# Performance work log

Hardware: AMD Instinct MI355X
Metric: run time of the kernel (lower is better)

Reference implementation:

```python
import jax, jax.numpy as jnp
import numpy as np

# Sizes: N nodes, E edges, C channels (atoms/node), CF channel_nf, R relations,
# H hidden/feature dim (uniform across the 2 AM_EGCL layers), L layers.
N, E, C, CF, R, H, L = 10000, 160000, 4, 16, 7, 256, 2
EPS = 1e-5


def setup_inputs() -> dict:
    key = jax.random.key(0)
    ks = jax.random.split(key, 16)
    p = lambda k, shape: (jax.random.normal(k, shape, jnp.float32) * 0.02)
    inp = {
        "input": jax.random.normal(ks[0], (N, H), jnp.float32),
        "coords": jax.random.normal(ks[1], (N, C, 3), jnp.float32),
        "channel_attr": jax.random.normal(ks[2], (N, C, CF), jnp.float32),
        # strictly positive channel weights (atom-occupancy style)
        "channel_weights": jax.random.uniform(ks[3], (N, C), jnp.float32) + 0.5,
        "edge_weights": jax.random.uniform(ks[4], (E,), jnp.float32),
    }
    src = jax.random.randint(ks[5], (E,), 0, N)
    dst = jax.random.randint(ks[6], (E,), 0, N)
    rel = jax.random.randint(ks[7], (E,), 0, R)
    inp["edge_list"] = jnp.stack([src, dst, rel], axis=1)
    ein = 2 * H + CF + 2 * CF  # h_i, h_j, radial feat, pooled channel attr i/j
    inp.update({
        "W_rad": p(ks[8], (L, C * C, CF)), "b_rad": jnp.zeros((L, CF), jnp.float32),
        "W_e1": p(ks[9], (L, ein, H)), "b_e1": jnp.zeros((L, H), jnp.float32),
        "W_e2": p(ks[10], (L, H, H)), "b_e2": jnp.zeros((L, H), jnp.float32),
        "W_c1": p(ks[11], (L, H, H)), "b_c1": jnp.zeros((L, H), jnp.float32),
        "W_c2": p(ks[12], (L, H, C * C)),
        "W_n1": p(ks[13], (L, R * H + H, H)), "b_n1": jnp.zeros((L, H), jnp.float32),
        "W_n2": p(ks[14], (L, H, H)), "b_n2": jnp.zeros((L, H), jnp.float32),
        "ln_g": jnp.ones((L, H), jnp.float32), "ln_b": jnp.zeros((L, H), jnp.float32),
    })
    return inp


def _am_egcl(h, x, edge_list, channel_attr, channel_weights, edge_weights, prm):
    """One adaptive multichannel equivariant graph conv layer."""
    (W_rad, b_rad, W_e1, b_e1, W_e2, b_e2, W_c1, b_c1, W_c2,
     W_n1, b_n1, W_n2, b_n2, ln_g, ln_b) = prm
    row, col, rel = edge_list[:, 0], edge_list[:, 1], edge_list[:, 2]
    # --- multichannel invariant radial features -------------------------------
    xd = x[row][:, :, None, :] - x[col][:, None, :, :]        # [E,C,C,3]
    radial = jnp.sum(xd * xd, axis=-1)                         # [E,C,C]
    wmask = channel_weights[row][:, :, None] * channel_weights[col][:, None, :]
    radial = radial * wmask
    rad_feat = jax.nn.silu(radial.reshape(-1, C * C) @ W_rad + b_rad)  # [E,CF]
    # pooled (weighted-mean) channel attribute per node
    csum = jnp.sum(channel_weights, axis=-1, keepdims=True)
    ca = jnp.sum(channel_attr * channel_weights[..., None], axis=1) / csum  # [N,CF]
    # --- edge message MLP ------------------------------------------------------
    m_in = jnp.concatenate([h[row], h[col], rad_feat, ca[row], ca[col]], axis=-1)
    m = jax.nn.silu(jax.nn.silu(m_in @ W_e1 + b_e1) @ W_e2 + b_e2)  # [E,H]
    m = m * edge_weights[:, None]
    # --- equivariant coord update ---------------------------------------------
    phi = (jax.nn.silu(m @ W_c1 + b_c1) @ W_c2).reshape(-1, C, C)   # [E,C,C]
    trans = jnp.mean(xd * phi[..., None], axis=2)                   # [E,C,3]
    ones = jnp.ones((trans.shape[0],), x.dtype)
    cnt = jnp.maximum(jax.ops.segment_sum(ones, row, num_segments=N), 1.0)
    x_out = x + jax.ops.segment_sum(trans, row, num_segments=N) / cnt[:, None, None]
    # --- relational node aggregation (GearNet-style, per-relation bins) --------
    seg = col * R + rel
    agg = jax.ops.segment_sum(m, seg, num_segments=N * R).reshape(N, R * H)
    h_out = jax.nn.silu(jnp.concatenate([agg, h], axis=-1) @ W_n1 + b_n1) @ W_n2 + b_n2
    # dropout p=0 (eval) -> identity; then LayerNorm
    mu = jnp.mean(h_out, axis=-1, keepdims=True)
    var = jnp.var(h_out, axis=-1, keepdims=True)
    h_out = (h_out - mu) * jax.lax.rsqrt(var + EPS) * ln_g + ln_b
    return h_out, x_out


def reference(input, edge_list, coords, channel_attr, channel_weights, edge_weights,
              W_rad, b_rad, W_e1, b_e1, W_e2, b_e2, W_c1, b_c1, W_c2,
              W_n1, b_n1, W_n2, b_n2, ln_g, ln_b):
    h, x = input, coords
    for i in range(L):  # fixed small layer count
        prm = (W_rad[i], b_rad[i], W_e1[i], b_e1[i], W_e2[i], b_e2[i],
               W_c1[i], b_c1[i], W_c2[i], W_n1[i], b_n1[i], W_n2[i], b_n2[i],
               ln_g[i], ln_b[i])
        h, x = _am_egcl(h, x, edge_list, channel_attr, channel_weights,
                        edge_weights, prm)
    return h, x  # (node_feature [N,H], coord_feature [N,C,3])
```

## Files before the change

### kernel.cpp

```cpp
#include <hip/hip_runtime.h>
#include <hip/hip_bf16.h>

#define NN 10000
#define EE 160000
#define CCH 4
#define CF 16
#define RR 7
#define HH 256
#define NSEG 70000
#define SCB 274
#define EPSV 1e-5f

typedef unsigned short ushort_t;
typedef __bf16 bf16x8 __attribute__((ext_vector_type(8)));
typedef float f32x4 __attribute__((ext_vector_type(4)));

__device__ __forceinline__ float silu_f(float v) {
    float e = __builtin_amdgcn_exp2f(v * -1.442695040888963f);
    return v * __builtin_amdgcn_rcpf(1.f + e);
}

__device__ __forceinline__ ushort_t bf16u_m(float f) {
    unsigned int u = __builtin_bit_cast(unsigned int, f);
    u += 0x7fffu + ((u >> 16) & 1u);
    return (ushort_t)(u >> 16);
}

__device__ __forceinline__ ushort_t bf16u_n(float f) {
    return __builtin_bit_cast(ushort_t, (__bf16)f);
}

__device__ __forceinline__ float ubf2f(ushort_t u) {
    unsigned int v = ((unsigned int)u) << 16;
    return __builtin_bit_cast(float, v);
}


__device__ __forceinline__ void pack_tile(
    const float* __restrict__ W, ushort_t* __restrict__ out,
    int Kreal, int N, int kt, int nt, int NTOT, int lane)
{
    int n = nt * 16 + (lane & 15);
    int kbase = kt * 32 + (lane >> 4) * 8;
    ushort_t* o = out + ((size_t)(kt * NTOT + nt) * 64 + lane) * 8;
    #pragma unroll
    for (int j = 0; j < 8; ++j) {
        int k = kbase + j;
        o[j] = (k < Kreal) ? bf16u_n(W[(size_t)k * N + n]) : (ushort_t)0;
    }
}

__device__ __forceinline__ void pack_ab_tile(
    const float* __restrict__ W_e1, ushort_t* __restrict__ pab,
    int kt, int nt, int lane)
{
    int nl = nt * 16 + (lane & 15);
    int kbase = kt * 32 + (lane >> 4) * 8;
    ushort_t* o = pab + ((size_t)(kt * 32 + nt) * 64 + lane) * 8;
    #pragma unroll
    for (int j = 0; j < 8; ++j) {
        int k = kbase + j;
        float v = 0.f;
        if (k < 256) {
            v = (nl < 256) ? W_e1[(size_t)k * 256 + nl]
                           : W_e1[(size_t)(256 + k) * 256 + (nl - 256)];
        } else if (k < 272) {
            int kk = k - 256;
            v = (nl < 256) ? W_e1[(size_t)(528 + kk) * 256 + nl]
                           : W_e1[(size_t)(544 + kk) * 256 + (nl - 256)];
        }
        o[j] = bf16u_n(v);
    }
}

__device__ __forceinline__ void pack_e1c_tile(
    const float* __restrict__ W_e1, ushort_t* __restrict__ pe1c,
    int nt, int lane)
{
    int n = nt * 16 + (lane & 15);
    int kbase = (lane >> 4) * 8;
    ushort_t* o = pe1c + ((size_t)nt * 64 + lane) * 8;
    #pragma unroll
    for (int j = 0; j < 8; ++j) {
        int k = kbase + j;
        o[j] = (k < 16) ? bf16u_n(W_e1[(size_t)(512 + k) * 256 + n]) : (ushort_t)0;
    }
}

__device__ __forceinline__ void pack_dispatch(
    int c, int lane,
    const float* __restrict__ W_e1, const float* __restrict__ W_e2,
    const float* __restrict__ W_c1, const float* __restrict__ W_c2,
    const float* __restrict__ W_n1, const float* __restrict__ W_n2,
    ushort_t* __restrict__ pab, ushort_t* __restrict__ pe1c,
    ushort_t* __restrict__ pe2,
    ushort_t* __restrict__ pc1, ushort_t* __restrict__ pc2,
    ushort_t* __restrict__ pn1, ushort_t* __restrict__ pn2)
{
    int l = 0;
    if (c >= 1720) { l = 1; c -= 1720; }
    const float* We1 = W_e1 + (size_t)l * 143360;
    if (c < 288) {
        pack_ab_tile(We1, pab + (size_t)l * 147456, c / 32, c % 32, lane);
    } else if (c < 304) {
        pack_e1c_tile(We1, pe1c + (size_t)l * 8192, c - 288, lane);
    } else if (c < 432) {
        int d = c - 304;
        pack_tile(W_e2 + (size_t)l * 65536, pe2 + (size_t)l * 65536,
                  256, 256, d / 16, d & 15, 16, lane);
    } else if (c < 560) {
        int d = c - 432;
        pack_tile(W_c1 + (size_t)l * 65536, pc1 + (size_t)l * 65536,
                  256, 256, d / 16, d & 15, 16, lane);
    } else if (c < 568) {
        int d = c - 560;
        pack_tile(W_c2 + (size_t)l * 4096, pc2 + (size_t)l * 4096,
                  256, 16, d, 0, 1, lane);
    } else if (c < 1592) {
        int d = c - 568;
        pack_tile(W_n1 + (size_t)l * 524288, pn1 + (size_t)l * 524288,
                  2048, 256, d / 16, d & 15, 16, lane);
    } else {
        int d = c - 1592;
        pack_tile(W_n2 + (size_t)l * 65536, pn2 + (size_t)l * 65536,
                  256, 256, d / 16, d & 15, 16, lane);
    }
}


__global__ __launch_bounds__(256) void prep_kernel(
    const float* __restrict__ input, ushort_t* __restrict__ hb16,
    const float* __restrict__ attr, const float* __restrict__ cw,
    ushort_t* __restrict__ cab16,
    int* __restrict__ hist, int* __restrict__ cursor,
    float* __restrict__ deg, float* __restrict__ xacc,
    const float* __restrict__ W_e1, const float* __restrict__ W_e2,
    const float* __restrict__ W_c1, const float* __restrict__ W_c2,
    const float* __restrict__ W_n1, const float* __restrict__ W_n2,
    ushort_t* __restrict__ pab, ushort_t* __restrict__ pe1c,
    ushort_t* __restrict__ pe2,
    ushort_t* __restrict__ pc1, ushort_t* __restrict__ pc2,
    ushort_t* __restrict__ pn1, ushort_t* __restrict__ pn2)
{
    int b = blockIdx.x, tid = threadIdx.x;
    if (b < 10000) {
        int t = b * 256 + tid;
        hb16[t] = bf16u_n(input[t]);
    } else if (b < 10625) {
        int t = (b - 10000) * 256 + tid;
        int n = t >> 4, f = t & 15;
        float s = 0.f, cs = 0.f;
        #pragma unroll
        for (int c = 0; c < CCH; ++c) {
            float w = cw[n * CCH + c];
            s  += attr[(n * CCH + c) * CF + f] * w;
            cs += w;
        }
        cab16[t] = bf16u_n(s / cs);
    } else if (b < 10899) {
        int t = (b - 10625) * 256 + tid;
        if (t < NSEG) hist[t] = 0;
    } else if (b < 11173) {
        int t = (b - 10899) * 256 + tid;
        if (t < NSEG) cursor[t] = 0;
    } else if (b < 11213) {
        int t = (b - 11173) * 256 + tid;
        if (t < NN) deg[t] = 0.f;
    } else if (b < 11682) {
        int t = (b - 11213) * 256 + tid;
        if (t < NN * 12) xacc[t] = 0.f;
    } else {
        int c = (b - 11682) * 4 + (tid >> 6);
        pack_dispatch(c, tid & 63, W_e1, W_e2, W_c1, W_c2, W_n1, W_n2,
                      pab, pe1c, pe2, pc1, pc2, pn1, pn2);
    }
}

__global__ __launch_bounds__(256) void histdeg_kernel(
    const int* __restrict__ el, int* __restrict__ hist, float* __restrict__ deg)
{
    int e = blockIdx.x * 256 + threadIdx.x;
    if (e < EE) {
        int r = el[e * 3], c = el[e * 3 + 1], rl = el[e * 3 + 2];
        atomicAdd(&hist[c * RR + rl], 1);
        atomicAdd(&deg[r], 1.f);
    }
}

__global__ __launch_bounds__(256) void scan1_kernel(
    const int* __restrict__ hist, int* __restrict__ pscan, int* __restrict__ bsum)
{
    __shared__ int sc[256];
    int b = blockIdx.x, t = threadIdx.x, i = b * 256 + t;
    int v = (i < NSEG) ? hist[i] : 0;
    sc[t] = v; __syncthreads();
    for (int off = 1; off < 256; off <<= 1) {
        int u = (t >= off) ? sc[t - off] : 0;
        __syncthreads();
        sc[t] += u;
        __syncthreads();
    }
    if (i < NSEG) pscan[i] = sc[t] - v;
    if (t == 255) bsum[b] = sc[255];
}

__global__ __launch_bounds__(256) void scan2_kernel(
    const int* __restrict__ bsum, int* __restrict__ bofs, int nb)
{
    __shared__ int sc[512];
    int t = threadIdx.x;
    int o1 = (t < nb) ? bsum[t] : 0;
    int o2 = (t + 256 < nb) ? bsum[t + 256] : 0;
    sc[t] = o1; sc[t + 256] = o2;
    __syncthreads();
    for (int off = 1; off < 512; off <<= 1) {
        int u1 = (t >= off) ? sc[t - off] : 0;
        int u2 = (t + 256 >= off) ? sc[t + 256 - off] : 0;
        __syncthreads();
        sc[t] += u1; sc[t + 256] += u2;
        __syncthreads();
    }
    if (t < nb) bofs[t] = sc[t] - o1;
    if (t + 256 < nb) bofs[t + 256] = sc[t + 256] - o2;
}

__global__ __launch_bounds__(256) void scan3_kernel(
    const int* __restrict__ pscan, const int* __restrict__ bofs, int* __restrict__ segst)
{
    int b = blockIdx.x, t = threadIdx.x, i = b * 256 + t;
    if (i < NSEG) segst[i] = pscan[i] + bofs[b];
    if (i == 0) segst[NSEG] = EE;
}

__global__ __launch_bounds__(256) void scatter_kernel(
    const int* __restrict__ el, const int* __restrict__ segst,
    int* __restrict__ cursor, int* __restrict__ perm)
{
    int e = blockIdx.x * 256 + threadIdx.x;
    if (e < EE) {
        int s = el[e * 3 + 1] * RR + el[e * 3 + 2];
        int pos = segst[s] + atomicAdd(&cursor[s], 1);
        perm[pos] = e;
    }
}


__global__ __launch_bounds__(256, 3) void abk_kernel(
    const ushort_t* __restrict__ hb16, const ushort_t* __restrict__ cab16,
    const ushort_t* __restrict__ pab, const float* __restrict__ b_e1,
    ushort_t* __restrict__ A16, ushort_t* __restrict__ B16)
{
    __shared__ ushort_t inbuf[32][296];
    __shared__ ushort_t obuf[32][520];
    const int tid = threadIdx.x, lane = tid & 63, w = tid >> 6;
    const int ar = lane & 15, aq = (lane >> 4) * 8, quad = lane >> 4;
    const int n0 = blockIdx.x * 32;
    const uint4 z4 = {0u, 0u, 0u, 0u};

    #pragma unroll
    for (int it = 0; it < 4; ++it) {
        int c = it * 256 + tid;
        int e = c >> 5, i4 = c & 31;
        int node = n0 + e;
        uint4 v = (node < NN) ? ((const uint4*)(hb16 + (size_t)node * 256))[i4] : z4;
        *(uint4*)&inbuf[e][i4 * 8] = v;
    }
    if (tid < 64) {
        int e = tid >> 1, i4 = tid & 1;
        int node = n0 + e;
        uint4 v = (node < NN) ? ((const uint4*)(cab16 + node * 16))[i4] : z4;
        *(uint4*)&inbuf[e][256 + i4 * 8] = v;
    } else if (tid < 128) {
        int c = tid - 64, e = c >> 1, i4 = c & 1;
        *(uint4*)&inbuf[e][272 + i4 * 8] = z4;
    }
    __syncthreads();

    const f32x4 Z = {0.f, 0.f, 0.f, 0.f};
    f32x4 acc[2][8];
    #pragma unroll
    for (int mt = 0; mt < 2; ++mt)
        #pragma unroll
        for (int jt = 0; jt < 8; ++jt) acc[mt][jt] = Z;
    for (int kt = 0; kt < 9; ++kt) {
        bf16x8 a0 = *(const bf16x8*)&inbuf[ar][kt * 32 + aq];
        bf16x8 a1 = *(const bf16x8*)&inbuf[16 + ar][kt * 32 + aq];
        #pragma unroll
        for (int jt = 0; jt < 8; ++jt) {
            bf16x8 b = *(const bf16x8*)(pab + ((size_t)(kt * 32 + w * 8 + jt) * 64 + lane) * 8);
            acc[0][jt] = __builtin_amdgcn_mfma_f32_16x16x32_bf16(a0, b, acc[0][jt], 0, 0, 0);
            acc[1][jt] = __builtin_amdgcn_mfma_f32_16x16x32_bf16(a1, b, acc[1][jt], 0, 0, 0);
        }
    }
    #pragma unroll
    for (int jt = 0; jt < 8; ++jt) {
        int n = w * 128 + jt * 16 + ar;
        float bias = (n < 256) ? b_e1[n] : 0.f;
        #pragma unroll
        for (int mt = 0; mt < 2; ++mt)
            #pragma unroll
            for (int r = 0; r < 4; ++r)
                obuf[mt * 16 + quad * 4 + r][n] = bf16u_n(acc[mt][jt][r] + bias);
    }
    __syncthreads();
    #pragma unroll
    for (int it = 0; it < 8; ++it) {
        int c = it * 256 + tid;
        int e = c >> 6, i4 = c & 63;
        int node = n0 + e;
        if (node < NN) {
            if (i4 < 32)
                *(uint4*)(A16 + (size_t)node * 256 + i4 * 8) = *(const uint4*)&obuf[e][i4 * 8];
            else
                *(uint4*)(B16 + (size_t)node * 256 + (i4 - 32) * 8) = *(const uint4*)&obuf[e][256 + (i4 - 32) * 8];
        }
    }
}


template<int KT, int NTOT>
__device__ __forceinline__ void mfma_stage32(
    const ushort_t (&A)[32][584], int colOff,
    const ushort_t* __restrict__ Wp, int w, int lane,
    f32x4 (&acc)[2][4])
{
    const f32x4 Z = {0.f, 0.f, 0.f, 0.f};
    #pragma unroll
    for (int mt = 0; mt < 2; ++mt)
        #pragma unroll
        for (int j = 0; j < 4; ++j) acc[mt][j] = Z;
    const int ar = lane & 15, aq = (lane >> 4) * 8;
    for (int kt = 0; kt < KT; ++kt) {
        bf16x8 a0 = *(const bf16x8*)&A[ar][colOff + kt * 32 + aq];
        bf16x8 a1 = *(const bf16x8*)&A[16 + ar][colOff + kt * 32 + aq];
        #pragma unroll
        for (int j = 0; j < 4; ++j) {
            bf16x8 b = *(const bf16x8*)(Wp + ((size_t)(kt * NTOT + w * 4 + j) * 64 + lane) * 8);
            acc[0][j] = __builtin_amdgcn_mfma_f32_16x16x32_bf16(a0, b, acc[0][j], 0, 0, 0);
            acc[1][j] = __builtin_amdgcn_mfma_f32_16x16x32_bf16(a1, b, acc[1][j], 0, 0, 0);
        }
    }
}


__global__ __launch_bounds__(256, 4) void edge_kernel(
    const int* __restrict__ el, const int* __restrict__ perm,
    const float* __restrict__ cw,
    const float* __restrict__ ew, const float* __restrict__ x,
    const ushort_t* __restrict__ A16, const ushort_t* __restrict__ B16,
    const float* __restrict__ W_rad, const float* __restrict__ b_rad,
    const ushort_t* __restrict__ pe1c,
    const ushort_t* __restrict__ pe2, const float* __restrict__ b_e2,
    const ushort_t* __restrict__ pc1, const float* __restrict__ b_c1,
    const ushort_t* __restrict__ pc2,
    ushort_t* __restrict__ mb16, float* __restrict__ xacc)
{
    __shared__ ushort_t abuf[32][584];
    __shared__ float radbuf[32][16];
    __shared__ int rowS[32], colS[32];
    __shared__ float ewS[32];

    const int tid = threadIdx.x, lane = tid & 63, w = tid >> 6;
    const int ar = lane & 15, aq = (lane >> 4) * 8, quad = lane >> 4;
    const int e0 = blockIdx.x * 32;

    if (tid < 32) {
        int eg = perm[e0 + tid];
        rowS[tid] = el[eg * 3 + 0];
        colS[tid] = el[eg * 3 + 1];
        ewS[tid]  = ew[eg];
    }
    __syncthreads();

    #pragma unroll
    for (int it = 0; it < 4; ++it) {
        int c = it * 256 + tid;
        int e = c >> 5, i4 = c & 31;
        bf16x8 va = *(const bf16x8*)((const uint4*)(A16 + (size_t)rowS[e] * 256) + i4);
        bf16x8 vb = *(const bf16x8*)((const uint4*)(B16 + (size_t)colS[e] * 256) + i4);
        bf16x8 vs;
        #pragma unroll
        for (int j = 0; j < 8; ++j)
            vs[j] = (__bf16)((float)va[j] + (float)vb[j]);
        *(bf16x8*)&abuf[e][288 + i4 * 8] = vs;
    }
    #pragma unroll
    for (int it = 0; it < 2; ++it) {
        int t = it * 256 + tid;
        int e = t >> 4, ab = t & 15, a = ab >> 2, b = ab & 3;
        int row = rowS[e], col = colS[e];
        float d0 = x[row * 12 + a * 3 + 0] - x[col * 12 + b * 3 + 0];
        float d1 = x[row * 12 + a * 3 + 1] - x[col * 12 + b * 3 + 1];
        float d2 = x[row * 12 + a * 3 + 2] - x[col * 12 + b * 3 + 2];
        radbuf[e][ab] = (d0 * d0 + d1 * d1 + d2 * d2)
                      * cw[row * CCH + a] * cw[col * CCH + b];
    }
    __syncthreads();

    #pragma unroll
    for (int it = 0; it < 2; ++it) {
        int t = it * 256 + tid;
        int e = t >> 4, f = t & 15;
        float acc = b_rad[f];
        #pragma unroll
        for (int ab = 0; ab < 16; ++ab) acc += radbuf[e][ab] * W_rad[ab * 16 + f];
        abuf[e][f] = bf16u_m(silu_f(acc));
        abuf[e][16 + f] = 0;
    }
    __syncthreads();

    f32x4 acc[2][4];

    mfma_stage32<1, 16>(abuf, 0, pe1c, w, lane, acc);
    #pragma unroll
    for (int j = 0; j < 4; ++j) {
        int n = w * 64 + j * 16 + ar;
        #pragma unroll
        for (int mt = 0; mt < 2; ++mt)
            #pragma unroll
            for (int r = 0; r < 4; ++r) {
                int e = mt * 16 + quad * 4 + r;
                float s = ubf2f(abuf[e][288 + n]) + acc[mt][j][r];
                abuf[e][288 + n] = bf16u_m(silu_f(s));
            }
    }
    __syncthreads();

    mfma_stage32<8, 16>(abuf, 288, pe2, w, lane, acc);
    #pragma unroll
    for (int j = 0; j < 4; ++j) {
        int n = w * 64 + j * 16 + ar;
        float bj = b_e2[n];
        #pragma unroll
        for (int mt = 0; mt < 2; ++mt)
            #pragma unroll
            for (int r = 0; r < 4; ++r) {
                int e = mt * 16 + quad * 4 + r;
                abuf[e][n] = bf16u_m(silu_f(acc[mt][j][r] + bj) * ewS[e]);
            }
    }
    __syncthreads();

    #pragma unroll
    for (int it = 0; it < 4; ++it) {
        int t = it * 256 + tid;
        int e = t >> 5, c = t & 31;
        *(uint4*)(mb16 + ((size_t)(e0 + e) * 256 + c * 8)) =
            *(const uint4*)&abuf[e][c * 8];
    }

    mfma_stage32<8, 16>(abuf, 0, pc1, w, lane, acc);
    #pragma unroll
    for (int j = 0; j < 4; ++j) {
        int n = w * 64 + j * 16 + ar;
        float bj = b_c1[n];
        #pragma unroll
        for (int mt = 0; mt < 2; ++mt)
            #pragma unroll
            for (int r = 0; r < 4; ++r)
                abuf[mt * 16 + quad * 4 + r][288 + n] = bf16u_m(silu_f(acc[mt][j][r] + bj));
    }
    __syncthreads();

    if (w < 2) {
        const f32x4 Z = {0.f, 0.f, 0.f, 0.f};
        f32x4 p = Z;
        #pragma unroll
        for (int kt = 0; kt < 8; ++kt) {
            bf16x8 a = *(const bf16x8*)&abuf[w * 16 + ar][288 + kt * 32 + aq];
            bf16x8 b = *(const bf16x8*)(pc2 + ((size_t)kt * 64 + lane) * 8);
            p = __builtin_amdgcn_mfma_f32_16x16x32_bf16(a, b, p, 0, 0, 0);
        }
        #pragma unroll
        for (int r = 0; r < 4; ++r)
            radbuf[w * 16 + quad * 4 + r][ar] = p[r];
    }
    __syncthreads();

    for (int t = tid; t < 384; t += 256) {
        int e = t / 12, r = t - e * 12, a = r / 3, k = r - a * 3;
        int row = rowS[e], col = colS[e];
        float xr = x[row * 12 + a * 3 + k];
        float s = 0.f;
        #pragma unroll
        for (int b = 0; b < 4; ++b)
            s += (xr - x[col * 12 + b * 3 + k]) * radbuf[e][a * 4 + b];
        atomicAdd(&xacc[row * 12 + a * 3 + k], 0.25f * s);
    }
}


__global__ __launch_bounds__(256, 4) void node_kernel(
    const ushort_t* __restrict__ mb16, const int* __restrict__ segst,
    const ushort_t* __restrict__ pn1, const float* __restrict__ b_n1,
    const ushort_t* __restrict__ pn2, const float* __restrict__ b_n2,
    const float* __restrict__ ln_g, const float* __restrict__ ln_b,
    float* __restrict__ h_out, ushort_t* __restrict__ hb16,
    const float* __restrict__ x_in, float* __restrict__ xacc,
    const float* __restrict__ deg, float* __restrict__ x_out)
{
    __shared__ __align__(16) char arena[33024];
    __shared__ float redS[16][16], red2S[16][16], muS[16], rsS[16];
    ushort_t (*nbuf)[1032] = (ushort_t(*)[1032])arena;
    ushort_t (*tbuf)[264] = (ushort_t(*)[264])arena;
    float (*h2buf)[264] = (float(*)[264])(arena + 8448);

    const int tid = threadIdx.x, lane = tid & 63, w = tid >> 6;
    const int n0 = blockIdx.x * 16;
    const int ar = lane & 15, aq = (lane >> 4) * 8;
    const f32x4 Z = {0.f, 0.f, 0.f, 0.f};

    if (tid < 192) {
        int ln = tid / 12, r = tid - ln * 12;
        int n = n0 + ln;
        float c = fmaxf(deg[n], 1.f);
        x_out[n * 12 + r] = x_in[n * 12 + r] + xacc[n * 12 + r] / c;
        xacc[n * 12 + r] = 0.f;
    }

    f32x4 acc[4] = {Z, Z, Z, Z};
    for (int chunk = 0; chunk < 2; ++chunk) {
        for (int ln = 0; ln < 4; ++ln) {
            int node = w * 4 + ln;
            int gnode = n0 + node;
            if (chunk == 0) {
                #pragma unroll
                for (int r = 0; r < 4; ++r) {
                    int s = gnode * RR + r;
                    int beg = segst[s], end = segst[s + 1];
                    float a0 = 0.f, a1 = 0.f, a2 = 0.f, a3 = 0.f;
                    for (int e = beg; e < end; ++e) {
                        ushort4 u = *(const ushort4*)(mb16 + (size_t)e * 256 + lane * 4);
                        a0 += ubf2f(u.x); a1 += ubf2f(u.y);
                        a2 += ubf2f(u.z); a3 += ubf2f(u.w);
                    }
                    ushort4 o;
                    o.x = bf16u_n(a0); o.y = bf16u_n(a1); o.z = bf16u_n(a2); o.w = bf16u_n(a3);
                    *(ushort4*)&nbuf[node][r * 256 + lane * 4] = o;
                }
            } else {
                #pragma unroll
                for (int r = 4; r < 7; ++r) {
                    int s = gnode * RR + r;
                    int beg = segst[s], end = segst[s + 1];
                    float a0 = 0.f, a1 = 0.f, a2 = 0.f, a3 = 0.f;
                    for (int e = beg; e < end; ++e) {
                        ushort4 u = *(const ushort4*)(mb16 + (size_t)e * 256 + lane * 4);
                        a0 += ubf2f(u.x); a1 += ubf2f(u.y);
                        a2 += ubf2f(u.z); a3 += ubf2f(u.w);
                    }
                    ushort4 o;
                    o.x = bf16u_n(a0); o.y = bf16u_n(a1); o.z = bf16u_n(a2); o.w = bf16u_n(a3);
                    *(ushort4*)&nbuf[node][(r - 4) * 256 + lane * 4] = o;
                }
                *(ushort4*)&nbuf[node][768 + lane * 4] =
                    *(const ushort4*)(hb16 + (size_t)gnode * 256 + lane * 4);
            }
        }
        __syncthreads();
        for (int kt = 0; kt < 32; ++kt) {
            bf16x8 a = *(const bf16x8*)&nbuf[ar][kt * 32 + aq];
            int ktg = chunk * 32 + kt;
            #pragma unroll
            for (int j = 0; j < 4; ++j) {
                bf16x8 b = *(const bf16x8*)(pn1 + ((size_t)(ktg * 16 + w * 4 + j) * 64 + lane) * 8);
                acc[j] = __builtin_amdgcn_mfma_f32_16x16x32_bf16(a, b, acc[j], 0, 0, 0);
            }
        }
        __syncthreads();
    }
    #pragma unroll
    for (int j = 0; j < 4; ++j) {
        int n = w * 64 + j * 16 + ar;
        float bj = b_n1[n];
        #pragma unroll
        for (int r = 0; r < 4; ++r)
            tbuf[(lane >> 4) * 4 + r][n] = bf16u_n(silu_f(acc[j][r] + bj));
    }
    __syncthreads();
    f32x4 acc2[4] = {Z, Z, Z, Z};
    for (int kt = 0; kt < 8; ++kt) {
        bf16x8 a = *(const bf16x8*)&tbuf[ar][kt * 32 + aq];
        #pragma unroll
        for (int j = 0; j < 4; ++j) {
            bf16x8 b = *(const bf16x8*)(pn2 + ((size_t)(kt * 16 + w * 4 + j) * 64 + lane) * 8);
            acc2[j] = __builtin_amdgcn_mfma_f32_16x16x32_bf16(a, b, acc2[j], 0, 0, 0);
        }
    }
    float hv[4][4];
    #pragma unroll
    for (int j = 0; j < 4; ++j) {
        int n = w * 64 + j * 16 + ar;
        float bj = b_n2[n];
        #pragma unroll
        for (int r = 0; r < 4; ++r) {
            hv[j][r] = acc2[j][r] + bj;
            h2buf[(lane >> 4) * 4 + r][n] = hv[j][r];
        }
    }
    __syncthreads();
    {
        int node = tid >> 4, c = tid & 15;
        float s = 0.f, s2 = 0.f;
        #pragma unroll
        for (int i = 0; i < 16; ++i) {
            float v = h2buf[node][c * 16 + i];
            s += v; s2 += v * v;
        }
        redS[node][c] = s; red2S[node][c] = s2;
    }
    __syncthreads();
    if (tid < 16) {
        float s = 0.f, s2 = 0.f;
        #pragma unroll
        for (int c = 0; c < 16; ++c) { s += redS[tid][c]; s2 += red2S[tid][c]; }
        float mu = s * (1.f / 256.f);
        muS[tid] = mu;
        rsS[tid] = rsqrtf(s2 * (1.f / 256.f) - mu * mu + EPSV);
    }
    __syncthreads();
    #pragma unroll
    for (int j = 0; j < 4; ++j) {
        int n = w * 64 + j * 16 + ar;
        float g = ln_g[n], bb = ln_b[n];
        #pragma unroll
        for (int r = 0; r < 4; ++r) {
            int row = (lane >> 4) * 4 + r;
            float v = (hv[j][r] - muS[row]) * rsS[row] * g + bb;
            if (h_out) h_out[(size_t)(n0 + row) * HH + n] = v;
            hb16[(size_t)(n0 + row) * HH + n] = bf16u_n(v);
        }
    }
}


extern "C" void kernel_launch(void* const* d_in, const int* in_sizes, int n_in,
                              void* d_out, int out_size, void* d_ws, size_t ws_size,
                              hipStream_t stream)
{
    const float* input  = (const float*)d_in[0];
    const float* coords = (const float*)d_in[1];
    const float* cattr  = (const float*)d_in[2];
    const float* cwts   = (const float*)d_in[3];
    const float* ewts   = (const float*)d_in[4];
    const int*   elist  = (const int*)d_in[5];
    const float* W_rad  = (const float*)d_in[6];
    const float* b_rad  = (const float*)d_in[7];
    const float* W_e1   = (const float*)d_in[8];
    const float* b_e1   = (const float*)d_in[9];
    const float* W_e2   = (const float*)d_in[10];
    const float* b_e2   = (const float*)d_in[11];
    const float* W_c1   = (const float*)d_in[12];
    const float* b_c1   = (const float*)d_in[13];
    const float* W_c2   = (const float*)d_in[14];
    const float* W_n1   = (const float*)d_in[15];
    const float* b_n1   = (const float*)d_in[16];
    const float* W_n2   = (const float*)d_in[17];
    const float* b_n2   = (const float*)d_in[18];
    const float* ln_g   = (const float*)d_in[19];
    const float* ln_b   = (const float*)d_in[20];

    float* wsf  = (float*)d_ws;
    float* deg  = wsf;
    float* xacc = deg + 10000;
    float* xbuf = xacc + 120000;
    int* ip     = (int*)(xbuf + 120000);
    int* hist   = ip;
    int* pscan  = hist + 70000;
    int* cursor = pscan + 70000;
    int* segst  = cursor + 70000;
    int* bsum   = segst + 70001;
    int* bofs   = bsum + 512;
    int* perm   = bofs + 512;
    ushort_t* up = (ushort_t*)(((uintptr_t)(perm + 160000) + 15) & ~(uintptr_t)15);
    ushort_t* hb16  = up;
    ushort_t* cab16 = hb16 + 2560000;
    ushort_t* mb16  = cab16 + 160000;
    ushort_t* A16   = mb16 + 40960000;
    ushort_t* B16   = A16 + 2560000;
    ushort_t* pab   = B16 + 2560000;
    ushort_t* pe1c  = pab + 294912;
    ushort_t* pe2   = pe1c + 16384;
    ushort_t* pc1   = pe2 + 131072;
    ushort_t* pc2   = pc1 + 131072;
    ushort_t* pn1   = pc2 + 8192;
    ushort_t* pn2   = pn1 + 1048576;

    prep_kernel<<<12542, 256, 0, stream>>>(
        input, hb16, cattr, cwts, cab16, hist, cursor, deg, xacc,
        W_e1, W_e2, W_c1, W_c2, W_n1, W_n2,
        pab, pe1c, pe2, pc1, pc2, pn1, pn2);

    histdeg_kernel<<<(EE + 255) / 256, 256, 0, stream>>>(elist, hist, deg);
    scan1_kernel<<<SCB, 256, 0, stream>>>(hist, pscan, bsum);
    scan2_kernel<<<1, 256, 0, stream>>>(bsum, bofs, SCB);
    scan3_kernel<<<SCB, 256, 0, stream>>>(pscan, bofs, segst);
    scatter_kernel<<<(EE + 255) / 256, 256, 0, stream>>>(elist, segst, cursor, perm);

    for (int l = 0; l < 2; ++l) {
        const float* x_in = (l == 0) ? coords : xbuf;
        float* h_out = (l == 0) ? nullptr : (float*)d_out;
        float* x_out = (l == 0) ? xbuf : ((float*)d_out + (size_t)NN * HH);

        abk_kernel<<<(NN + 31) / 32, 256, 0, stream>>>(
            hb16, cab16, pab + (size_t)l * 147456, b_e1 + l * HH, A16, B16);

        edge_kernel<<<EE / 32, 256, 0, stream>>>(
            elist, perm, cwts, ewts, x_in, A16, B16,
            W_rad + l * 256, b_rad + l * 16,
            pe1c + (size_t)l * 8192,
            pe2 + (size_t)l * 65536,  b_e2 + l * HH,
            pc1 + (size_t)l * 65536,  b_c1 + l * HH,
            pc2 + (size_t)l * 4096,
            mb16, xacc);

        node_kernel<<<NN / 16, 256, 0, stream>>>(
            mb16, segst,
            pn1 + (size_t)l * 524288, b_n1 + l * HH,
            pn2 + (size_t)l * 65536,  b_n2 + l * HH,
            ln_g + l * HH, ln_b + l * HH,
            h_out, hb16,
            x_in, xacc, deg, x_out);
    }
}
```

Measured before the change: 508.6 us.

## Fuse next-layer A/B edge-projection precompute into node kernel epilogue

The layer-1 abk_kernel launch is removed. Its per-node projection of [h, pooled channel attr] through W_e1 into A16/B16 is now computed inside node_kernel right after LayerNorm, using the bf16 h values already held in shared memory. This saves one kernel launch and the re-read of hb16 from global memory. In exchange node_kernel gains an extra MFMA phase, more shared-memory reuse of the arena, and an extra barrier, which may add register pressure.

Measured after the change: 497.4 us (median of 2 runs). 2.2% less time.

```diff
diff --git a/kernel.cpp b/kernel.cpp
--- a/kernel.cpp
+++ b/kernel.cpp
@@ -497,17 +497,22 @@
     const float* __restrict__ ln_g, const float* __restrict__ ln_b,
     float* __restrict__ h_out, ushort_t* __restrict__ hb16,
     const float* __restrict__ x_in, float* __restrict__ xacc,
-    const float* __restrict__ deg, float* __restrict__ x_out)
+    const float* __restrict__ deg, float* __restrict__ x_out,
+    const ushort_t* __restrict__ cab16,
+    const ushort_t* __restrict__ pabn, const float* __restrict__ b_e1n,
+    ushort_t* __restrict__ A16, ushort_t* __restrict__ B16)
 {
     __shared__ __align__(16) char arena[33024];
     __shared__ float redS[16][16], red2S[16][16], muS[16], rsS[16];
     ushort_t (*nbuf)[1032] = (ushort_t(*)[1032])arena;
     ushort_t (*tbuf)[264] = (ushort_t(*)[264])arena;
     float (*h2buf)[264] = (float(*)[264])(arena + 8448);
+    ushort_t (*habuf)[296] = (ushort_t(*)[296])arena;
+    ushort_t (*obuf)[520] = (ushort_t(*)[520])(arena + 9472);
 
     const int tid = threadIdx.x, lane = tid & 63, w = tid >> 6;
     const int n0 = blockIdx.x * 16;
-    const int ar = lane & 15, aq = (lane >> 4) * 8;
+    const int ar = lane & 15, aq = (lane >> 4) * 8, quad = lane >> 4;
     const f32x4 Z = {0.f, 0.f, 0.f, 0.f};
 
     if (tid < 192) {
@@ -628,7 +633,47 @@
             int row = (lane >> 4) * 4 + r;
             float v = (hv[j][r] - muS[row]) * rsS[row] * g + bb;
             if (h_out) h_out[(size_t)(n0 + row) * HH + n] = v;
-            hb16[(size_t)(n0 + row) * HH + n] = bf16u_n(v);
+            ushort_t hb = bf16u_n(v);
+            hb16[(size_t)(n0 + row) * HH + n] = hb;
+            if (pabn) habuf[row][n] = hb;
+        }
+    }
+
+    if (pabn) {
+        if (tid < 256) {
+            int node = tid >> 4, f = tid & 15;
+            habuf[node][256 + f] = cab16[(n0 + node) * 16 + f];
+            habuf[node][272 + f] = 0;
+        }
+        __syncthreads();
+        f32x4 pacc[8] = {Z, Z, Z, Z, Z, Z, Z, Z};
+        for (int kt = 0; kt < 9; ++kt) {
+            bf16x8 a = *(const bf16x8*)&habuf[ar][kt * 32 + aq];
+            #pragma unroll
+            for (int jt = 0; jt < 8; ++jt) {
+                bf16x8 b = *(const bf16x8*)(pabn + ((size_t)(kt * 32 + w * 8 + jt) * 64 + lane) * 8);
+                pacc[jt] = __builtin_amdgcn_mfma_f32_16x16x32_bf16(a, b, pacc[jt], 0, 0, 0);
+            }
+        }
+        #pragma unroll
+        for (int jt = 0; jt < 8; ++jt) {
+            int n = w * 128 + jt * 16 + ar;
+            float bias = (n < 256) ? b_e1n[n] : 0.f;
+            #pragma unroll
+            for (int r = 0; r < 4; ++r)
+                obuf[quad * 4 + r][n] = bf16u_n(pacc[jt][r] + bias);
+        }
+        __syncthreads();
+        #pragma unroll
+        for (int it = 0; it < 4; ++it) {
+            int c = it * 256 + tid;
+            int node = c >> 6, i4 = c & 63;
+            if (i4 < 32)
+                *(uint4*)(A16 + (size_t)(n0 + node) * 256 + i4 * 8) =
+                    *(const uint4*)&obuf[node][i4 * 8];
+            else
+                *(uint4*)(B16 + (size_t)(n0 + node) * 256 + (i4 - 32) * 8) =
+                    *(const uint4*)&obuf[node][256 + (i4 - 32) * 8];
         }
     }
 }
@@ -697,13 +742,13 @@
     scan3_kernel<<<SCB, 256, 0, stream>>>(pscan, bofs, segst);
     scatter_kernel<<<(EE + 255) / 256, 256, 0, stream>>>(elist, segst, cursor, perm);
 
+    abk_kernel<<<(NN + 31) / 32, 256, 0, stream>>>(
+        hb16, cab16, pab, b_e1, A16, B16);
+
     for (int l = 0; l < 2; ++l) {
         const float* x_in = (l == 0) ? coords : xbuf;
         float* h_out = (l == 0) ? nullptr : (float*)d_out;
         float* x_out = (l == 0) ? xbuf : ((float*)d_out + (size_t)NN * HH);
-
-        abk_kernel<<<(NN + 31) / 32, 256, 0, stream>>>(
-            hb16, cab16, pab + (size_t)l * 147456, b_e1 + l * HH, A16, B16);
 
         edge_kernel<<<EE / 32, 256, 0, stream>>>(
             elist, perm, cwts, ewts, x_in, A16, B16,
@@ -720,6 +765,10 @@
             pn2 + (size_t)l * 65536,  b_n2 + l * HH,
             ln_g + l * HH, ln_b + l * HH,
             h_out, hb16,
-            x_in, xacc, deg, x_out);
-    }
-}
+            x_in, xacc, deg, x_out,
+            cab16,
+            (l == 0) ? (pab + 147456) : nullptr,
+            (l == 0) ? (b_e1 + HH) : nullptr,
+            A16, B16);
+    }
+}
```
